# Kernel tuning notes

Measured on AMD Instinct MI355X. Metric: run time of the kernel, lower is better.

The kernel has to match this reference:

```python
import jax, jax.numpy as jnp
import numpy as np

B, NQ, NK = 8, 1024, 1024
DQ = DK = DV = 512
H = 8
DH = DV // H
EPS = 1e-5
NEG = -1e9


def _layer_norm(x, g, b):
    mu = jnp.mean(x, axis=-1, keepdims=True)
    var = jnp.mean(jnp.square(x - mu), axis=-1, keepdims=True)
    return (x - mu) * jax.lax.rsqrt(var + EPS) * g + b


def setup_inputs() -> dict:
    key = jax.random.key(0)
    ks = jax.random.split(key, 16)
    s_q = 1.0 / np.sqrt(DQ)
    s_k = 1.0 / np.sqrt(DK)
    s_v = 1.0 / np.sqrt(DV)
    return {
        "Q": jax.random.normal(ks[0], (B, NQ, DQ), jnp.float32),
        "K": jax.random.normal(ks[1], (B, NK, DK), jnp.float32),
        "mask": jax.random.randint(ks[2], (B, NK), 0, 2, jnp.int32),
        "Wq": jax.random.uniform(ks[3], (DQ, DV), jnp.float32, -s_q, s_q),
        "bq": jax.random.uniform(ks[4], (DV,), jnp.float32, -s_q, s_q),
        "Wk": jax.random.uniform(ks[5], (DK, DV), jnp.float32, -s_k, s_k),
        "bk": jax.random.uniform(ks[6], (DV,), jnp.float32, -s_k, s_k),
        "Wv": jax.random.uniform(ks[7], (DK, DV), jnp.float32, -s_k, s_k),
        "bv": jax.random.uniform(ks[8], (DV,), jnp.float32, -s_k, s_k),
        "Wo": jax.random.uniform(ks[9], (DV, DV), jnp.float32, -s_v, s_v),
        "bo": jax.random.uniform(ks[10], (DV,), jnp.float32, -s_v, s_v),
        "g0": jnp.ones((DV,), jnp.float32),
        "b0": jnp.zeros((DV,), jnp.float32),
        "g1": jnp.ones((DV,), jnp.float32),
        "b1": jnp.zeros((DV,), jnp.float32),
    }


def reference(Q, K, mask, Wq, bq, Wk, bk, Wv, bv, Wo, bo, g0, b0, g1, b1):
    b = Q.shape[0]
    # projections: [B, N, DV] -> [B, N, H, DH]
    q = (Q @ Wq + bq).reshape(b, -1, H, DH)
    k = (K @ Wk + bk).reshape(b, -1, H, DH)
    v = (K @ Wv + bv).reshape(b, -1, H, DH)
    scores = jnp.einsum("bqhd,bkhd->bhqk", q, k) / np.sqrt(DH)  # [B,H,Nq,Nk]
    scores = jnp.where((mask == 0)[:, None, None, :], NEG, scores)
    A = jax.nn.softmax(scores, axis=-1)
    o = q + jnp.einsum("bhqk,bkhd->bqhd", A, v)  # residual on projected Q (per head)
    O = o.reshape(b, -1, DV)
    O = _layer_norm(O, g0, b0)
    O = O + jax.nn.relu(O @ Wo + bo)
    O = _layer_norm(O, g1, b1)
    return O
```

## Files before the change

### kernel.cpp

```cpp
#include <hip/hip_runtime.h>


typedef float f32x4 __attribute__((ext_vector_type(4)));
typedef short bf16x8 __attribute__((ext_vector_type(8)));
typedef unsigned short u16;

#define MFMA16 __builtin_amdgcn_mfma_f32_16x16x32_bf16

__device__ __forceinline__ float bf2f(u16 u){
    unsigned x = ((unsigned)u) << 16;
    return __builtin_bit_cast(float, x);
}
__device__ __forceinline__ u16 f2bf(float f){
    unsigned u = __builtin_bit_cast(unsigned, f);
    u = u + 0x7fffu + ((u >> 16) & 1u);
    return (u16)(u >> 16);
}

__global__ __launch_bounds__(256) void transpose_w(
    const float* __restrict__ Wq, const float* __restrict__ Wk,
    const float* __restrict__ Wv, const float* __restrict__ Wo,
    u16* __restrict__ wt)
{
    const int z = blockIdx.z;
    const float* W = (z == 0) ? Wq : (z == 1) ? Wk : (z == 2) ? Wv : Wo;
    u16* out = wt + (size_t)z * 512 * 512;

    __shared__ u16 tile[32][33];
    const int k0 = blockIdx.y * 32, n0 = blockIdx.x * 32;
    const int c = threadIdx.x & 31, r = threadIdx.x >> 5;
#pragma unroll
    for (int i = 0; i < 4; i++) {
        int rr = r + i * 8;
        tile[rr][c] = f2bf(W[(size_t)(k0 + rr) * 512 + n0 + c]);
    }
    __syncthreads();
#pragma unroll
    for (int i = 0; i < 4; i++) {
        int rr = r + i * 8;
        out[(size_t)(n0 + rr) * 512 + k0 + c] = tile[c][rr];
    }
}

__global__ __launch_bounds__(256) void transpose_v(
    const u16* __restrict__ vb, u16* __restrict__ vtg)
{
    __shared__ u16 tile[32][33];
    const int bh = blockIdx.z;
    const int b = bh >> 3, h = bh & 7;
    const int k0 = blockIdx.x * 32, d0 = blockIdx.y * 32;
    const int c = threadIdx.x & 31, r = threadIdx.x >> 5;
#pragma unroll
    for (int i = 0; i < 4; i++) {
        int rr = r + i * 8;
        tile[rr][c] = vb[(size_t)(b * 1024 + k0 + rr) * 512 + h * 64 + d0 + c];
    }
    __syncthreads();
#pragma unroll
    for (int i = 0; i < 4; i++) {
        int rr = r + i * 8;
        vtg[(size_t)(bh * 64 + d0 + rr) * 1024 + k0 + c] = tile[c][rr];
    }
}

__global__ __launch_bounds__(256) void gemm_proj(
    const float* __restrict__ Q, const float* __restrict__ K,
    const u16* __restrict__ wt,
    const float* __restrict__ bq, const float* __restrict__ bk, const float* __restrict__ bv,
    u16* __restrict__ qb, u16* __restrict__ kb, u16* __restrict__ vb)
{
    __shared__ __align__(16) u16 lds_a[128 * 40];
    __shared__ __align__(16) u16 lds_b[128 * 40];

    const int z = blockIdx.z;
    const float* X = (z == 0) ? Q : K;
    const u16* Wt = wt + (size_t)z * 512 * 512;
    const float* bias = (z == 0) ? bq : (z == 1) ? bk : bv;
    u16* outb = (z == 0) ? qb : (z == 1) ? kb : vb;

    const int bm = blockIdx.y, bn = blockIdx.x;
    const int t = threadIdx.x;
    const int wave = t >> 6, lane = t & 63, quad = lane >> 4, lm = lane & 15;
    const int wm = wave >> 1, wn = wave & 1;

    f32x4 acc[4][4];
    const f32x4 zz = {0.f, 0.f, 0.f, 0.f};
#pragma unroll
    for (int i = 0; i < 4; i++)
#pragma unroll
        for (int j = 0; j < 4; j++) acc[i][j] = zz;

    for (int k0 = 0; k0 < 512; k0 += 32) {
#pragma unroll
        for (int i = 0; i < 2; i++) {
            int idx = t + i * 256;
            int r = idx >> 2, c = (idx & 3) * 8;
            const float* xp = &X[(size_t)(bm * 128 + r) * 512 + k0 + c];
            f32x4 a0 = *(const f32x4*)xp;
            f32x4 a1 = *(const f32x4*)(xp + 4);
            bf16x8 xv;
#pragma unroll
            for (int j = 0; j < 4; j++) { xv[j] = (short)f2bf(a0[j]); xv[4 + j] = (short)f2bf(a1[j]); }
            *(bf16x8*)&lds_a[r * 40 + c] = xv;
            *(bf16x8*)&lds_b[r * 40 + c] =
                *(const bf16x8*)&Wt[(size_t)(bn * 128 + r) * 512 + k0 + c];
        }
        __syncthreads();
        bf16x8 af[4], bfr[4];
#pragma unroll
        for (int mi = 0; mi < 4; mi++)
            af[mi] = *(const bf16x8*)&lds_a[(wm * 64 + mi * 16 + lm) * 40 + quad * 8];
#pragma unroll
        for (int ni = 0; ni < 4; ni++)
            bfr[ni] = *(const bf16x8*)&lds_b[(wn * 64 + ni * 16 + lm) * 40 + quad * 8];
#pragma unroll
        for (int mi = 0; mi < 4; mi++)
#pragma unroll
            for (int ni = 0; ni < 4; ni++)
                acc[mi][ni] = MFMA16(af[mi], bfr[ni], acc[mi][ni], 0, 0, 0);
        __syncthreads();
    }

#pragma unroll
    for (int mi = 0; mi < 4; mi++) {
#pragma unroll
        for (int ni = 0; ni < 4; ni++) {
            const int col = bn * 128 + wn * 64 + ni * 16 + lm;
            const float bv_ = bias[col];
#pragma unroll
            for (int r = 0; r < 4; r++) {
                const int row = bm * 128 + wm * 64 + mi * 16 + quad * 4 + r;
                outb[(size_t)row * 512 + col] = f2bf(acc[mi][ni][r] + bv_);
            }
        }
    }
}

__global__ __launch_bounds__(256) void gemm_mlp(
    const u16* __restrict__ X, const u16* __restrict__ wt,
    const float* __restrict__ bo, const float* __restrict__ resid,
    float* __restrict__ outf)
{
    __shared__ __align__(16) u16 lds_a[128 * 40];
    __shared__ __align__(16) u16 lds_b[128 * 40];

    const u16* Wt = wt + (size_t)3 * 512 * 512;
    const int bm = blockIdx.y, bn = blockIdx.x;
    const int t = threadIdx.x;
    const int wave = t >> 6, lane = t & 63, quad = lane >> 4, lm = lane & 15;
    const int wm = wave >> 1, wn = wave & 1;

    f32x4 acc[4][4];
    const f32x4 zz = {0.f, 0.f, 0.f, 0.f};
#pragma unroll
    for (int i = 0; i < 4; i++)
#pragma unroll
        for (int j = 0; j < 4; j++) acc[i][j] = zz;

    for (int k0 = 0; k0 < 512; k0 += 32) {
#pragma unroll
        for (int i = 0; i < 2; i++) {
            int idx = t + i * 256;
            int r = idx >> 2, c = (idx & 3) * 8;
            *(bf16x8*)&lds_a[r * 40 + c] =
                *(const bf16x8*)&X[(size_t)(bm * 128 + r) * 512 + k0 + c];
            *(bf16x8*)&lds_b[r * 40 + c] =
                *(const bf16x8*)&Wt[(size_t)(bn * 128 + r) * 512 + k0 + c];
        }
        __syncthreads();
        bf16x8 af[4], bfr[4];
#pragma unroll
        for (int mi = 0; mi < 4; mi++)
            af[mi] = *(const bf16x8*)&lds_a[(wm * 64 + mi * 16 + lm) * 40 + quad * 8];
#pragma unroll
        for (int ni = 0; ni < 4; ni++)
            bfr[ni] = *(const bf16x8*)&lds_b[(wn * 64 + ni * 16 + lm) * 40 + quad * 8];
#pragma unroll
        for (int mi = 0; mi < 4; mi++)
#pragma unroll
            for (int ni = 0; ni < 4; ni++)
                acc[mi][ni] = MFMA16(af[mi], bfr[ni], acc[mi][ni], 0, 0, 0);
        __syncthreads();
    }

#pragma unroll
    for (int mi = 0; mi < 4; mi++) {
#pragma unroll
        for (int ni = 0; ni < 4; ni++) {
            const int col = bn * 128 + wn * 64 + ni * 16 + lm;
            const float bv_ = bo[col];
#pragma unroll
            for (int r = 0; r < 4; r++) {
                const int row = bm * 128 + wm * 64 + mi * 16 + quad * 4 + r;
                const size_t off = (size_t)row * 512 + col;
                outf[off] = resid[off] + fmaxf(acc[mi][ni][r] + bv_, 0.f);
            }
        }
    }
}

__global__ __launch_bounds__(256, 4) void attn_kernel(
    const u16* __restrict__ qb, const u16* __restrict__ kb, const u16* __restrict__ vtg,
    const int* __restrict__ mask, float* __restrict__ O)
{
    __shared__ __align__(16) u16 k_tile[64 * 88];
    __shared__ __align__(16) u16 vt[64 * 88];
    __shared__ __align__(16) u16 p_st[4 * 16 * 88];
    __shared__ float mbias[1024];

    const int i = blockIdx.x;
    const int s_ = i >> 3;
    const int bh = (i & 7) + 8 * (s_ >> 4);
    const int qt = s_ & 15;
    const int b = bh >> 3, h = bh & 7;

    const int t = threadIdx.x, wave = t >> 6, lane = t & 63;
    const int quad = lane >> 4, lm = lane & 15;
    const int qbase = qt * 64 + wave * 16;
    const size_t baseb = (size_t)b * 1024 * 512;
    const size_t vbase = (size_t)((b * 8 + h) * 64) * 1024;

#pragma unroll
    for (int ii = 0; ii < 4; ii++) {
        int j = t + ii * 256;
        mbias[j] = mask[b * 1024 + j] ? 0.0f : -30000.0f;
    }

    bf16x8 aq[2];
#pragma unroll
    for (int ks = 0; ks < 2; ks++)
        aq[ks] = *(const bf16x8*)&qb[baseb +
            (size_t)(qbase + lm) * 512 + h * 64 + ks * 32 + quad * 8];

    float lsum[4] = {0.f, 0.f, 0.f, 0.f};
    f32x4 oacc[4];
    const f32x4 zz = {0.f, 0.f, 0.f, 0.f};
#pragma unroll
    for (int c = 0; c < 4; c++) oacc[c] = zz;

    const float SC2 = 0.125f * 1.44269504088896341f;
    const int srow = t >> 2, scol = (t & 3) * 16;
    u16* pw = &p_st[wave * 16 * 88];

    const u16* kgp = &kb[baseb + (size_t)srow * 512 + h * 64 + scol];
    const u16* vgp = &vtg[vbase + (size_t)srow * 1024 + scol];

    bf16x8 kA0, kA1, vA0, vA1, kB0, kB1, vB0, vB1;

    auto load_t = [&](int kt, bf16x8& k0, bf16x8& k1, bf16x8& v0, bf16x8& v1) {
        const u16* kp = kgp + (size_t)kt * 64 * 512;
        k0 = *(const bf16x8*)kp;
        k1 = *(const bf16x8*)(kp + 8);
        const u16* vp = vgp + kt * 64;
        v0 = *(const bf16x8*)vp;
        v1 = *(const bf16x8*)(vp + 8);
    };
    auto store_t = [&](bf16x8 k0, bf16x8 k1, bf16x8 v0, bf16x8 v1) {
        *(bf16x8*)&k_tile[srow * 88 + scol]     = k0;
        *(bf16x8*)&k_tile[srow * 88 + scol + 8] = k1;
        *(bf16x8*)&vt[srow * 88 + scol]     = v0;
        *(bf16x8*)&vt[srow * 88 + scol + 8] = v1;
    };

    auto compute_t = [&](int kt) {
        const int keyg = kt * 64;
        bf16x8 bk[4][2];
#pragma unroll
        for (int n = 0; n < 4; n++)
#pragma unroll
            for (int ks = 0; ks < 2; ks++)
                bk[n][ks] = *(const bf16x8*)&k_tile[(n * 16 + lm) * 88 + ks * 32 + quad * 8];

#pragma unroll
        for (int n = 0; n < 4; n++) {
            f32x4 S = zz;
            __builtin_amdgcn_s_setprio(1);
            S = MFMA16(aq[0], bk[n][0], S, 0, 0, 0);
            S = MFMA16(aq[1], bk[n][1], S, 0, 0, 0);
            __builtin_amdgcn_s_setprio(0);
            const float bias = mbias[keyg + n * 16 + lm];
#pragma unroll
            for (int r = 0; r < 4; r++) {
                float p = __builtin_amdgcn_exp2f(__builtin_fmaf(S[r], SC2, bias));
                lsum[r] += p;
                pw[(quad * 4 + r) * 88 + n * 16 + lm] = f2bf(p);
            }
        }

#pragma unroll
        for (int ks = 0; ks < 2; ks++) {
            bf16x8 ap = *(const bf16x8*)&pw[lm * 88 + ks * 32 + quad * 8];
            __builtin_amdgcn_s_setprio(1);
#pragma unroll
            for (int c = 0; c < 4; c++) {
                bf16x8 bv_ = *(const bf16x8*)&vt[(c * 16 + lm) * 88 + ks * 32 + quad * 8];
                oacc[c] = MFMA16(ap, bv_, oacc[c], 0, 0, 0);
            }
            __builtin_amdgcn_s_setprio(0);
        }
    };

    load_t(0, kA0, kA1, vA0, vA1);

    for (int kt = 0; kt < 16; kt += 2) {
        store_t(kA0, kA1, vA0, vA1);
        load_t(kt + 1, kB0, kB1, vB0, vB1);
        __syncthreads();
        compute_t(kt);
        __syncthreads();
        store_t(kB0, kB1, vB0, vB1);
        load_t((kt + 2) & 15, kA0, kA1, vA0, vA1);
        __syncthreads();
        compute_t(kt + 1);
        __syncthreads();
    }

#pragma unroll
    for (int r = 0; r < 4; r++) {
        float s = lsum[r];
        s += __shfl_xor(s, 1); s += __shfl_xor(s, 2);
        s += __shfl_xor(s, 4); s += __shfl_xor(s, 8);
        lsum[r] = s;
    }

#pragma unroll
    for (int c = 0; c < 4; c++)
#pragma unroll
        for (int r = 0; r < 4; r++) {
            const int row = qbase + quad * 4 + r;
            const int d = h * 64 + c * 16 + lm;
            const size_t off = baseb + (size_t)row * 512 + d;
            O[off] = bf2f(qb[off]) + oacc[c][r] / lsum[r];
        }
}

__global__ __launch_bounds__(256) void ln_kernel(
    const float* __restrict__ in, const float* __restrict__ g, const float* __restrict__ bsh,
    u16* __restrict__ outb, float* __restrict__ outf)
{
    const int row = blockIdx.x * 4 + (threadIdx.x >> 6);
    const int lane = threadIdx.x & 63;
    const float* x = in + (size_t)row * 512 + lane * 8;
    float v[8];
    *(f32x4*)&v[0] = *(const f32x4*)&x[0];
    *(f32x4*)&v[4] = *(const f32x4*)&x[4];
    float s = 0.f, sq = 0.f;
#pragma unroll
    for (int j = 0; j < 8; j++) { s += v[j]; sq += v[j] * v[j]; }
#pragma unroll
    for (int off = 1; off < 64; off <<= 1) {
        s += __shfl_xor(s, off);
        sq += __shfl_xor(sq, off);
    }
    const float mu = s * (1.f / 512.f);
    const float var = sq * (1.f / 512.f) - mu * mu;
    const float rs = rsqrtf(var + 1e-5f);
    float y[8];
#pragma unroll
    for (int j = 0; j < 8; j++) {
        int col = lane * 8 + j;
        y[j] = (v[j] - mu) * rs * g[col] + bsh[col];
    }
    if (outb != nullptr) {
        bf16x8 ov;
#pragma unroll
        for (int j = 0; j < 8; j++) ov[j] = (short)f2bf(y[j]);
        *(bf16x8*)&outb[(size_t)row * 512 + lane * 8] = ov;
    }
    if (outf != nullptr) {
        float* o = outf + (size_t)row * 512 + lane * 8;
        *(f32x4*)&o[0] = *(const f32x4*)&y[0];
        *(f32x4*)&o[4] = *(const f32x4*)&y[4];
    }
}

extern "C" void kernel_launch(void* const* d_in, const int* in_sizes, int n_in,
                              void* d_out, int out_size, void* d_ws, size_t ws_size,
                              hipStream_t stream) {
    const float* Q  = (const float*)d_in[0];
    const float* K  = (const float*)d_in[1];
    const int* mask = (const int*)d_in[2];
    const float* Wq = (const float*)d_in[3];
    const float* bq = (const float*)d_in[4];
    const float* Wk = (const float*)d_in[5];
    const float* bk = (const float*)d_in[6];
    const float* Wv = (const float*)d_in[7];
    const float* bv = (const float*)d_in[8];
    const float* Wo = (const float*)d_in[9];
    const float* bo = (const float*)d_in[10];
    const float* g0 = (const float*)d_in[11];
    const float* b0 = (const float*)d_in[12];
    const float* g1 = (const float*)d_in[13];
    const float* b1 = (const float*)d_in[14];
    float* out = (float*)d_out;

    char* ws = (char*)d_ws;
    const size_t MB = 1048576;
    u16*   wt  = (u16*)(ws);
    u16*   qb  = (u16*)(ws + 2 * MB);
    u16*   kb  = (u16*)(ws + 10 * MB);
    u16*   vtg = (u16*)(ws + 18 * MB);
    u16*   vb  = (u16*)(ws + 26 * MB);
    float* Of  = (float*)(ws + 26 * MB);
    u16*   O1b = (u16*)(ws + 2 * MB);
    float* O1f = (float*)(ws + 10 * MB);
    float* Uf  = (float*)(ws + 26 * MB);

    transpose_w<<<dim3(16, 16, 4), 256, 0, stream>>>(Wq, Wk, Wv, Wo, wt);
    gemm_proj<<<dim3(4, 64, 3), 256, 0, stream>>>(Q, K, wt, bq, bk, bv, qb, kb, vb);
    transpose_v<<<dim3(32, 2, 64), 256, 0, stream>>>(vb, vtg);
    attn_kernel<<<1024, 256, 0, stream>>>(qb, kb, vtg, mask, Of);
    ln_kernel<<<2048, 256, 0, stream>>>(Of, g0, b0, O1b, O1f);
    gemm_mlp<<<dim3(4, 64, 1), 256, 0, stream>>>(O1b, wt, bo, O1f, Uf);
    ln_kernel<<<2048, 256, 0, stream>>>(Uf, g1, b1, nullptr, out);
}
```

Measured before the change: 207.4 us.

## Use direct global-to-LDS loads with XOR swizzle in GEMMs; read mask from global in attention

```diff
diff --git a/kernel.cpp b/kernel.cpp
--- a/kernel.cpp
+++ b/kernel.cpp
@@ -15,6 +15,12 @@
     unsigned u = __builtin_bit_cast(unsigned, f);
     u = u + 0x7fffu + ((u >> 16) & 1u);
     return (u16)(u >> 16);
+}
+
+__device__ __forceinline__ void gload_lds16(const u16* g, u16* l){
+    __builtin_amdgcn_global_load_lds(
+        (const __attribute__((address_space(1))) void*)g,
+        (__attribute__((address_space(3))) void*)l, 16, 0, 0);
 }
 
 __global__ __launch_bounds__(256) void transpose_w(
@@ -70,7 +76,7 @@
     u16* __restrict__ qb, u16* __restrict__ kb, u16* __restrict__ vb)
 {
     __shared__ __align__(16) u16 lds_a[128 * 40];
-    __shared__ __align__(16) u16 lds_b[128 * 40];
+    __shared__ __align__(16) u16 lds_b[128 * 32];
 
     const int z = blockIdx.z;
     const float* X = (z == 0) ? Q : K;
@@ -83,6 +89,16 @@
     const int wave = t >> 6, lane = t & 63, quad = lane >> 4, lm = lane & 15;
     const int wm = wave >> 1, wn = wave & 1;
 
+    const u16* bsrc[2];
+    u16* bdst[2];
+#pragma unroll
+    for (int j = 0; j < 2; j++) {
+        const int r = j * 64 + wave * 16 + (lane >> 2);
+        const int cg = ((lane & 3) ^ (r & 3)) * 8;
+        bsrc[j] = &Wt[(size_t)(bn * 128 + r) * 512 + cg];
+        bdst[j] = &lds_b[(j * 2048) + wave * 512];
+    }
+
     f32x4 acc[4][4];
     const f32x4 zz = {0.f, 0.f, 0.f, 0.f};
 #pragma unroll
@@ -91,6 +107,8 @@
         for (int j = 0; j < 4; j++) acc[i][j] = zz;
 
     for (int k0 = 0; k0 < 512; k0 += 32) {
+        gload_lds16(bsrc[0] + k0, bdst[0]);
+        gload_lds16(bsrc[1] + k0, bdst[1]);
 #pragma unroll
         for (int i = 0; i < 2; i++) {
             int idx = t + i * 256;
@@ -102,8 +120,6 @@
 #pragma unroll
             for (int j = 0; j < 4; j++) { xv[j] = (short)f2bf(a0[j]); xv[4 + j] = (short)f2bf(a1[j]); }
             *(bf16x8*)&lds_a[r * 40 + c] = xv;
-            *(bf16x8*)&lds_b[r * 40 + c] =
-                *(const bf16x8*)&Wt[(size_t)(bn * 128 + r) * 512 + k0 + c];
         }
         __syncthreads();
         bf16x8 af[4], bfr[4];
@@ -112,7 +128,8 @@
             af[mi] = *(const bf16x8*)&lds_a[(wm * 64 + mi * 16 + lm) * 40 + quad * 8];
 #pragma unroll
         for (int ni = 0; ni < 4; ni++)
-            bfr[ni] = *(const bf16x8*)&lds_b[(wn * 64 + ni * 16 + lm) * 40 + quad * 8];
+            bfr[ni] = *(const bf16x8*)&lds_b[(wn * 64 + ni * 16 + lm) * 32
+                                            + ((quad ^ (lm & 3)) * 8)];
 #pragma unroll
         for (int mi = 0; mi < 4; mi++)
 #pragma unroll
@@ -141,8 +158,8 @@
     const float* __restrict__ bo, const float* __restrict__ resid,
     float* __restrict__ outf)
 {
-    __shared__ __align__(16) u16 lds_a[128 * 40];
-    __shared__ __align__(16) u16 lds_b[128 * 40];
+    __shared__ __align__(16) u16 lds_a[128 * 32];
+    __shared__ __align__(16) u16 lds_b[128 * 32];
 
     const u16* Wt = wt + (size_t)3 * 512 * 512;
     const int bm = blockIdx.y, bn = blockIdx.x;
@@ -150,6 +167,20 @@
     const int wave = t >> 6, lane = t & 63, quad = lane >> 4, lm = lane & 15;
     const int wm = wave >> 1, wn = wave & 1;
 
+    const u16* asrc[2];
+    const u16* bsrc[2];
+    u16* adst[2];
+    u16* bdst[2];
+#pragma unroll
+    for (int j = 0; j < 2; j++) {
+        const int r = j * 64 + wave * 16 + (lane >> 2);
+        const int cg = ((lane & 3) ^ (r & 3)) * 8;
+        asrc[j] = &X [(size_t)(bm * 128 + r) * 512 + cg];
+        bsrc[j] = &Wt[(size_t)(bn * 128 + r) * 512 + cg];
+        adst[j] = &lds_a[(j * 2048) + wave * 512];
+        bdst[j] = &lds_b[(j * 2048) + wave * 512];
+    }
+
     f32x4 acc[4][4];
     const f32x4 zz = {0.f, 0.f, 0.f, 0.f};
 #pragma unroll
@@ -158,23 +189,19 @@
         for (int j = 0; j < 4; j++) acc[i][j] = zz;
 
     for (int k0 = 0; k0 < 512; k0 += 32) {
-#pragma unroll
-        for (int i = 0; i < 2; i++) {
-            int idx = t + i * 256;
-            int r = idx >> 2, c = (idx & 3) * 8;
-            *(bf16x8*)&lds_a[r * 40 + c] =
-                *(const bf16x8*)&X[(size_t)(bm * 128 + r) * 512 + k0 + c];
-            *(bf16x8*)&lds_b[r * 40 + c] =
-                *(const bf16x8*)&Wt[(size_t)(bn * 128 + r) * 512 + k0 + c];
-        }
+        gload_lds16(asrc[0] + k0, adst[0]);
+        gload_lds16(asrc[1] + k0, adst[1]);
+        gload_lds16(bsrc[0] + k0, bdst[0]);
+        gload_lds16(bsrc[1] + k0, bdst[1]);
         __syncthreads();
         bf16x8 af[4], bfr[4];
+        const int cxor = (quad ^ (lm & 3)) * 8;
 #pragma unroll
         for (int mi = 0; mi < 4; mi++)
-            af[mi] = *(const bf16x8*)&lds_a[(wm * 64 + mi * 16 + lm) * 40 + quad * 8];
+            af[mi] = *(const bf16x8*)&lds_a[(wm * 64 + mi * 16 + lm) * 32 + cxor];
 #pragma unroll
         for (int ni = 0; ni < 4; ni++)
-            bfr[ni] = *(const bf16x8*)&lds_b[(wn * 64 + ni * 16 + lm) * 40 + quad * 8];
+            bfr[ni] = *(const bf16x8*)&lds_b[(wn * 64 + ni * 16 + lm) * 32 + cxor];
 #pragma unroll
         for (int mi = 0; mi < 4; mi++)
 #pragma unroll
@@ -206,7 +233,6 @@
     __shared__ __align__(16) u16 k_tile[64 * 88];
     __shared__ __align__(16) u16 vt[64 * 88];
     __shared__ __align__(16) u16 p_st[4 * 16 * 88];
-    __shared__ float mbias[1024];
 
     const int i = blockIdx.x;
     const int s_ = i >> 3;
@@ -219,12 +245,7 @@
     const int qbase = qt * 64 + wave * 16;
     const size_t baseb = (size_t)b * 1024 * 512;
     const size_t vbase = (size_t)((b * 8 + h) * 64) * 1024;
-
-#pragma unroll
-    for (int ii = 0; ii < 4; ii++) {
-        int j = t + ii * 256;
-        mbias[j] = mask[b * 1024 + j] ? 0.0f : -30000.0f;
-    }
+    const int* mrow = &mask[b * 1024];
 
     bf16x8 aq[2];
 #pragma unroll
@@ -264,6 +285,11 @@
 
     auto compute_t = [&](int kt) {
         const int keyg = kt * 64;
+        float bias_n[4];
+#pragma unroll
+        for (int n = 0; n < 4; n++)
+            bias_n[n] = mrow[keyg + n * 16 + lm] ? 0.0f : -30000.0f;
+
         bf16x8 bk[4][2];
 #pragma unroll
         for (int n = 0; n < 4; n++)
@@ -278,10 +304,9 @@
             S = MFMA16(aq[0], bk[n][0], S, 0, 0, 0);
             S = MFMA16(aq[1], bk[n][1], S, 0, 0, 0);
             __builtin_amdgcn_s_setprio(0);
-            const float bias = mbias[keyg + n * 16 + lm];
 #pragma unroll
             for (int r = 0; r < 4; r++) {
-                float p = __builtin_amdgcn_exp2f(__builtin_fmaf(S[r], SC2, bias));
+                float p = __builtin_amdgcn_exp2f(__builtin_fmaf(S[r], SC2, bias_n[n]));
                 lsum[r] += p;
                 pw[(quad * 4 + r) * 88 + n * 16 + lm] = f2bf(p);
             }
```

Measured after the change: 206.4 us. No clear change (-0.5%).
